# Performance work log

Hardware: AMD Instinct MI355X
Metric: run time of the kernel (lower is better)

The kernel has to match this reference:

```python
import jax, jax.numpy as jnp
import numpy as np
from jax import lax

EPS = 1e-06
QP_ITERS = 500  # unrolled mirror-descent iterations for the simplex QP


def mlp_embed(x, W1, b1, W2, b2):
    # embedding_net: 2-layer MLP, [B, N, in_dim] -> [B, N, embed_dim]
    h = jax.nn.relu(jnp.einsum('bni,ih->bnh', x, W1) + b1)
    return jnp.einsum('bnh,hd->bnd', h, W2) + b2


def batch_svdd(emb, eps):
    # emb: [B, S, D].  SVDD dual QP per task:
    #   min_a  a^T K a - diag(K)^T a   s.t.  a >= 0, sum(a) = 1
    # (Q = 2K, p = -diag(K), G = -I, h = 0, A = 1^T, b = 1 in the torch QPFunction call)
    B, S, D = emb.shape
    K = jnp.einsum('bsd,btd->bst', emb, emb) + eps * jnp.eye(S, dtype=emb.dtype)
    kdiag = jnp.diagonal(K, axis1=-2, axis2=-1)  # [B, S]
    # Solve on the simplex with exponentiated-gradient (mirror descent with KL),
    # which converges to the unique QP optimum (K is PD after the eps jitter).
    # Per-task step size from the Gershgorin bound: eta <= 1 / (2 * ||K||_inf).
    eta = 1.0 / (2.0 * jnp.max(jnp.sum(jnp.abs(K), axis=-1), axis=-1, keepdims=True))  # [B,1]
    a0 = jnp.full((B, S), 1.0 / S, dtype=emb.dtype)

    def step(a, _):
        g = 2.0 * jnp.einsum('bst,bt->bs', K, a) - kdiag  # grad of a^T K a - kdiag^T a
        a = jax.nn.softmax(jnp.log(a + 1e-30) - eta * g, axis=-1)
        return a, None

    alphas, _ = lax.scan(step, a0, None, length=QP_ITERS)
    centers = jnp.einsum('bs,bsd->bd', alphas, emb)  # sum(alphas * inputs, dim=1)
    return centers


def setup_inputs() -> dict:
    key = jax.random.key(0)
    ks = jax.random.split(key, 4)
    tasks, shot, n_query, in_dim, hid, emb = 256, 32, 64, 1024, 2048, 512
    support_inputs = jax.random.normal(ks[0], (tasks, shot, in_dim), jnp.float32)
    query_inputs = jax.random.normal(ks[1], (tasks, n_query, in_dim), jnp.float32)
    W1 = jax.random.normal(ks[2], (in_dim, hid), jnp.float32) / np.sqrt(in_dim)
    b1 = jnp.zeros((hid,), jnp.float32)
    W2 = jax.random.normal(ks[3], (hid, emb), jnp.float32) / np.sqrt(hid)
    b2 = jnp.zeros((emb,), jnp.float32)
    return {'support_inputs': support_inputs, 'query_inputs': query_inputs,
            'W1': W1, 'b1': b1, 'W2': W2, 'b2': b2}


def reference(support_inputs, query_inputs, W1, b1, W2, b2):
    support_emb = mlp_embed(support_inputs, W1, b1, W2, b2)  # [B, S, D]
    centers = batch_svdd(support_emb, EPS)                   # [B, D]
    query_emb = mlp_embed(query_inputs, W1, b1, W2, b2)      # [B, Q, D]
    logits = -jnp.sum((centers[:, None, :] - query_emb) ** 2, axis=-1)  # [B, Q]
    return logits
```

## Files before the change

kernel.cpp:

```cpp
#include <hip/hip_runtime.h>
#include <hip/hip_bf16.h>

typedef __attribute__((ext_vector_type(8))) short bf16x8;
typedef __attribute__((ext_vector_type(4))) float f32x4;
typedef __attribute__((ext_vector_type(4))) unsigned short us4;

__device__ __forceinline__ unsigned short bf16_rne(float f) {
  unsigned u = __float_as_uint(f);
  unsigned r = u + 0x7fffu + ((u >> 16) & 1u);
  return (unsigned short)(r >> 16);
}

__device__ __forceinline__ void gload16(const void* g, void* l) {
  typedef const __attribute__((address_space(1))) unsigned int* gas;
  typedef __attribute__((address_space(3))) unsigned int* las;
  __builtin_amdgcn_global_load_lds((gas)g, (las)l, 16, 0, 0);
}

__device__ __forceinline__ float lane_f(float v, int l) {
  return __int_as_float(__builtin_amdgcn_readlane(__float_as_int(v), l));
}

template <int CTRL>
__device__ __forceinline__ float dpp_add(float x) {
  return x + __int_as_float(__builtin_amdgcn_update_dpp(0, __float_as_int(x), CTRL, 0xf, 0xf, true));
}

#define BAR() asm volatile("s_barrier" ::: "memory")
#define VMCNT0() asm volatile("s_waitcnt vmcnt(0)" ::: "memory")
#define LGKM4() asm volatile("s_waitcnt lgkmcnt(4)" ::: "memory")
#define LGKM0() asm volatile("s_waitcnt lgkmcnt(0)" ::: "memory")
#define SB() __builtin_amdgcn_sched_barrier(0)

__global__ __launch_bounds__(256) void castx(const float* __restrict__ sup,
                                             const float* __restrict__ qry,
                                             unsigned short* __restrict__ X) {
  const int stride = gridDim.x * blockDim.x;
  for (int i = blockIdx.x * blockDim.x + threadIdx.x; i < 6291456; i += stride) {
    float4 v = (i < 2097152) ? ((const float4*)sup)[i] : ((const float4*)qry)[i - 2097152];
    us4 o = { bf16_rne(v.x), bf16_rne(v.y), bf16_rne(v.z), bf16_rne(v.w) };
    *(us4*)(X + (size_t)i * 4) = o;
  }
}

__global__ __launch_bounds__(256) void transcast(const float* __restrict__ src,
                                                 unsigned short* __restrict__ dst,
                                                 int R, int C) {
  __shared__ float t[32][33];
  const int tx = threadIdx.x & 31, ty = threadIdx.x >> 5;
  const int c0 = blockIdx.x * 32, r0 = blockIdx.y * 32;
#pragma unroll
  for (int j = 0; j < 4; j++)
    t[ty + j * 8][tx] = src[(size_t)(r0 + ty + j * 8) * C + c0 + tx];
  __syncthreads();
#pragma unroll
  for (int j = 0; j < 4; j++)
    dst[(size_t)(c0 + ty + j * 8) * R + r0 + tx] = bf16_rne(t[tx][ty + j * 8]);
}

#define MFMA_Q(AO, BO, MOFF, NOFF)                                                  \
  __builtin_amdgcn_s_setprio(1);                                                    \
  _Pragma("unroll") for (int i_ = 0; i_ < 4; ++i_)                                  \
  _Pragma("unroll") for (int j_ = 0; j_ < 2; ++j_)                                  \
  _Pragma("unroll") for (int ks_ = 0; ks_ < 2; ++ks_)                               \
    acc[(MOFF) + i_][(NOFF) + j_] = __builtin_amdgcn_mfma_f32_16x16x32_bf16(        \
        AO[i_][ks_], BO[j_][ks_], acc[(MOFF) + i_][(NOFF) + j_], 0, 0, 0);          \
  __builtin_amdgcn_s_setprio(0);

#define RDA(KS, ACH, MH, I) \
  (*(const bf16x8*)(lsc + ((ACH) * 32768 + (MH) * 8192 + (I) * 2048) + ((KS) ? vA_1 : vA_0)))
#define RDB(KS, BCH, JI) \
  (*(const bf16x8*)(lsc + ((BCH) * 32768 + (JI) * 2048) + ((KS) ? vB_1 : vB_0)))

#define STG(GLP, CHOFF, HALF)                                                     \
  gload16((GLP) + (size_t)((HALF) * 128) * ld,                                    \
          (char*)ls + ((CHOFF) + (HALF) * 16384) + wid * 1024);                   \
  gload16((GLP) + (size_t)((HALF) * 128 + 64) * ld,                               \
          (char*)ls + ((CHOFF) + (HALF) * 16384 + 8192) + wid * 1024);

#define TILE(ACH, BCH, ASO, BSO, T)                                               \
  {                                                                               \
    VMCNT0();                                                                     \
    BAR();                                                                        \
    _Pragma("unroll") for (int i = 0; i < 4; ++i) {                               \
      afr[i][0] = RDA(0, ACH, 0, i); afr[i][1] = RDA(1, ACH, 0, i);               \
    }                                                                             \
    _Pragma("unroll") for (int j = 0; j < 2; ++j) {                               \
      bfr0[j][0] = RDB(0, BCH, j); bfr0[j][1] = RDB(1, BCH, j);                   \
    }                                                                             \
    _Pragma("unroll") for (int j = 0; j < 2; ++j) {                               \
      bfr1[j][0] = RDB(0, BCH, 2 + j); bfr1[j][1] = RDB(1, BCH, 2 + j);           \
    }                                                                             \
    const char* Ap_ = AgL + (size_t)(T) * 128;                                    \
    const char* Bp_ = BgL + (size_t)(T) * 128;                                    \
    STG(Ap_, ASO, 0); STG(Ap_, ASO, 1);                                           \
    STG(Bp_, BSO, 0); STG(Bp_, BSO, 1);                                           \
    LGKM4(); SB();                                                                \
    MFMA_Q(afr, bfr0, 0, 0);                                                      \
    LGKM0(); SB();                                                                \
    MFMA_Q(afr, bfr1, 0, 2);                                                      \
    _Pragma("unroll") for (int i = 0; i < 4; ++i) {                               \
      afr[i][0] = RDA(0, ACH, 1, i); afr[i][1] = RDA(1, ACH, 1, i);               \
    }                                                                             \
    LGKM0(); SB();                                                                \
    MFMA_Q(afr, bfr1, 4, 2);                                                      \
    MFMA_Q(afr, bfr0, 4, 0);                                                      \
  }

template <int ACT, int OUTBF>
__global__ __launch_bounds__(512) void gemm256(const unsigned short* __restrict__ A,
                                               const unsigned short* __restrict__ BT,
                                               const float* __restrict__ bias,
                                               void* __restrict__ Cout,
                                               int M, int N, int K) {
  __shared__ __attribute__((aligned(16))) short ls[4][16384];
  const int tid = threadIdx.x, lane = tid & 63, wid = tid >> 6;
  const int wm = wid >> 2, wn = wid & 3;
  const int l15 = lane & 15, lg = lane >> 4;

  int lin = blockIdx.y * gridDim.x + blockIdx.x;
  int nwg = gridDim.x * gridDim.y;
  int swz = (lin & 7) * (nwg >> 3) + (lin >> 3);
  int bx = swz % gridDim.x, by = swz / gridDim.x;
  const int m0 = by * 256, n0 = bx * 256;

  const size_t ld = (size_t)K * 2;
  const char* Ag = (const char*)A + (size_t)m0 * ld;
  const char* Bg = (const char*)BT + (size_t)n0 * ld;
  const int NT = K >> 6;
  const char* lsc = (const char*)ls;

  const int swz4 = (l15 & 7) << 4;
  const int bk0 = (l15 * 128 + lg * 16) ^ swz4;
  const int bk1 = (l15 * 128 + 64 + lg * 16) ^ swz4;
  const int vA_0 = bk0 + wm * 16384, vA_1 = bk1 + wm * 16384;
  const int vB_0 = bk0 + wn * 8192 + 65536, vB_1 = bk1 + wn * 8192 + 65536;

  const int srow = wid * 8 + (lane >> 3);
  const int kperm = ((lane & 7) ^ (lane >> 3)) << 4;
  const char* AgL = Ag + (size_t)srow * ld + kperm;
  const char* BgL = Bg + (size_t)srow * ld + kperm;

  f32x4 acc[8][4] = {};
  bf16x8 afr[4][2], bfr0[2][2], bfr1[2][2];

  STG(AgL, 0, 0); STG(AgL, 0, 1);
  STG(BgL, 65536, 0); STG(BgL, 65536, 1);

  for (int u = 0; u < NT; u += 2) {
    int t1 = u + 1;
    int t2 = u + 2; if (t2 >= NT) t2 = 0;
    TILE(0, 0, 32768, 98304, t1);
    TILE(1, 1, 0, 65536, t2);
  }

  float bv[4];
#pragma unroll
  for (int nf = 0; nf < 4; ++nf) bv[nf] = bias[n0 + wn * 64 + nf * 16 + l15];
#pragma unroll
  for (int mf = 0; mf < 8; ++mf) {
    int rbase = m0 + wm * 128 + mf * 16 + lg * 4;
#pragma unroll
    for (int nf = 0; nf < 4; ++nf) {
      int col = n0 + wn * 64 + nf * 16 + l15;
#pragma unroll
      for (int j = 0; j < 4; ++j) {
        float v = acc[mf][nf][j] + bv[nf];
        if (ACT) v = v > 0.f ? v : 0.f;
        size_t idx = (size_t)(rbase + j) * N + col;
        if (OUTBF) ((unsigned short*)Cout)[idx] = bf16_rne(v);
        else       ((float*)Cout)[idx] = v;
      }
    }
  }
}

template <int ACT, int OUTBF, int K>
__global__ __launch_bounds__(256, 3) void gemm2(const unsigned short* __restrict__ A,
                                                const unsigned short* __restrict__ BT,
                                                const float* __restrict__ bias,
                                                void* __restrict__ Cout,
                                                int N) {
  __shared__ __attribute__((aligned(16))) short ls[4][4096];
  const int tid = threadIdx.x, lane = tid & 63, wid = tid >> 6;
  const int wm = wid >> 1, wn = wid & 1;
  const int l15 = lane & 15, lg = lane >> 4;

  int lin = blockIdx.y * gridDim.x + blockIdx.x;
  int nwg = gridDim.x * gridDim.y;
  int swz = (lin & 7) * (nwg >> 3) + (lin >> 3);
  int bx = swz % gridDim.x, by = swz / gridDim.x;
  const int m0 = by * 128, n0 = bx * 128;

  constexpr size_t ldb = (size_t)K * 2;
  constexpr int NT = K >> 5;
  const char* Ag = (const char*)A + (size_t)m0 * ldb;
  const char* Bg = (const char*)BT + (size_t)n0 * ldb;
  char* lsw = (char*)ls;
  const char* lsc = (const char*)ls;

  const int vbase = l15 * 64 + ((lg ^ (l15 & 3)) << 4);
  const int vA = vbase + wm * 4096;
  const int vB = vbase + wn * 4096 + 16384;

  const int srow = wid * 16 + (lane >> 2);
  const int kperm = ((lane & 3) ^ ((lane >> 2) & 3)) << 4;
  const char* AgL = Ag + (size_t)srow * ldb + kperm;
  const char* BgL = Bg + (size_t)srow * ldb + kperm;

  f32x4 acc[4][4] = {};
  bf16x8 afr[4], bfr[4];

  auto STAGE = [&](const char* gl, int choff, int t) {
    gload16(gl + (size_t)t * 64, lsw + choff + wid * 1024);
    gload16(gl + 64 * ldb + (size_t)t * 64, lsw + choff + 4096 + wid * 1024);
  };

  auto TILE2 = [&](int ch, int oc, int tst) {
    VMCNT0();
    BAR();
#pragma unroll
    for (int i = 0; i < 4; ++i)
      afr[i] = *(const bf16x8*)(lsc + ch * 4096 + i * 1024 + vA);
#pragma unroll
    for (int nf = 0; nf < 4; ++nf)
      bfr[nf] = *(const bf16x8*)(lsc + ch * 4096 + nf * 1024 + vB);
    STAGE(AgL, oc * 4096, tst);
    STAGE(BgL, 16384 + oc * 4096, tst);
    __builtin_amdgcn_s_setprio(1);
#pragma unroll
    for (int nf = 0; nf < 4; ++nf)
#pragma unroll
      for (int i = 0; i < 4; ++i)
        acc[i][nf] = __builtin_amdgcn_mfma_f32_16x16x32_bf16(afr[i], bfr[nf],
                                                             acc[i][nf], 0, 0, 0);
    __builtin_amdgcn_s_setprio(0);
  };

  STAGE(AgL, 0, 0);
  STAGE(BgL, 16384, 0);
  for (int u = 0; u < NT; u += 2) {
    int t2 = u + 2; if (t2 >= NT) t2 = 0;
    TILE2(0, 1, u + 1);
    TILE2(1, 0, t2);
  }

  float bv[4];
#pragma unroll
  for (int nf = 0; nf < 4; ++nf) bv[nf] = bias[n0 + wn * 64 + nf * 16 + l15];
#pragma unroll
  for (int i = 0; i < 4; ++i) {
    int rbase = m0 + wm * 64 + i * 16 + lg * 4;
#pragma unroll
    for (int nf = 0; nf < 4; ++nf) {
      int col = n0 + wn * 64 + nf * 16 + l15;
#pragma unroll
      for (int j = 0; j < 4; ++j) {
        float v = acc[i][nf][j] + bv[nf];
        if (ACT) v = v > 0.f ? v : 0.f;
        size_t idx = (size_t)(rbase + j) * N + col;
        if (OUTBF) ((unsigned short*)Cout)[idx] = bf16_rne(v);
        else       ((float*)Cout)[idx] = v;
      }
    }
  }
}

__global__ __launch_bounds__(256) void makeK(const float* __restrict__ E,
                                             float* __restrict__ Km,
                                             float* __restrict__ eta2v) {
  __shared__ float es[32][512];
  const int b = blockIdx.x, tid = threadIdx.x;
  const float4* Eb = (const float4*)(E + (size_t)b * 32 * 512);
  float4* es4 = (float4*)&es[0][0];
  for (int i = tid; i < 32 * 128; i += 256) es4[i] = Eb[i];
  __syncthreads();

  const int s = tid >> 3, tq = tid & 7;
  const float4* rs4 = (const float4*)&es[s][0];
  const float4* rt0 = (const float4*)&es[tq * 4 + 0][0];
  const float4* rt1 = (const float4*)&es[tq * 4 + 1][0];
  const float4* rt2 = (const float4*)&es[tq * 4 + 2][0];
  const float4* rt3 = (const float4*)&es[tq * 4 + 3][0];
  float4 a0 = {0, 0, 0, 0}, a1 = {0, 0, 0, 0}, a2 = {0, 0, 0, 0}, a3 = {0, 0, 0, 0};
  for (int dd = 0; dd < 128; ++dd) {
    float4 av = rs4[dd];
    float4 b0 = rt0[dd], b1 = rt1[dd], b2 = rt2[dd], b3 = rt3[dd];
    a0.x = fmaf(av.x, b0.x, a0.x); a0.y = fmaf(av.y, b0.y, a0.y);
    a0.z = fmaf(av.z, b0.z, a0.z); a0.w = fmaf(av.w, b0.w, a0.w);
    a1.x = fmaf(av.x, b1.x, a1.x); a1.y = fmaf(av.y, b1.y, a1.y);
    a1.z = fmaf(av.z, b1.z, a1.z); a1.w = fmaf(av.w, b1.w, a1.w);
    a2.x = fmaf(av.x, b2.x, a2.x); a2.y = fmaf(av.y, b2.y, a2.y);
    a2.z = fmaf(av.z, b2.z, a2.z); a2.w = fmaf(av.w, b2.w, a2.w);
    a3.x = fmaf(av.x, b3.x, a3.x); a3.y = fmaf(av.y, b3.y, a3.y);
    a3.z = fmaf(av.z, b3.z, a3.z); a3.w = fmaf(av.w, b3.w, a3.w);
  }
  float kv[4] = { (a0.x + a0.y) + (a0.z + a0.w), (a1.x + a1.y) + (a1.z + a1.w),
                  (a2.x + a2.y) + (a2.z + a2.w), (a3.x + a3.y) + (a3.z + a3.w) };
  float p = 0.f;
#pragma unroll
  for (int j = 0; j < 4; j++) {
    if (s == tq * 4 + j) kv[j] += 1e-6f;
    p += fabsf(kv[j]);
    Km[(size_t)b * 1024 + s * 32 + tq * 4 + j] = kv[j];
  }
  p += __shfl_xor(p, 1); p += __shfl_xor(p, 2); p += __shfl_xor(p, 4);
  __syncthreads();
  float* rs = &es[0][0];
  if (tq == 0) rs[s] = p;
  __syncthreads();
  if (tid < 32) {
    float m = rs[tid];
    m = fmaxf(m, __shfl_xor(m, 1));
    m = fmaxf(m, __shfl_xor(m, 2));
    m = fmaxf(m, __shfl_xor(m, 4));
    m = fmaxf(m, __shfl_xor(m, 8));
    m = fmaxf(m, __shfl_xor(m, 16));
    if (tid == 0) eta2v[b] = 1.4426950408889634f / (2.0f * m);
  }
}

__global__ __launch_bounds__(256) void qp_kernel(const float* __restrict__ Km,
                                                 const float* __restrict__ eta2v,
                                                 float* __restrict__ alp) {
  const int lane = threadIdx.x & 63, wid = threadIdx.x >> 6;
  const int b = blockIdx.x * 4 + wid;
  const int s = lane & 31;
  const float* Kb = Km + (size_t)b * 1024;
  float kr[32];
#pragma unroll
  for (int i = 0; i < 8; i++) {
    float4 v = ((const float4*)(Kb + s * 32))[i];
    kr[i * 4 + 0] = v.x; kr[i * 4 + 1] = v.y; kr[i * 4 + 2] = v.z; kr[i * 4 + 3] = v.w;
  }
  const float kd = Kb[s * 33];
  const float eta2 = eta2v[b];
  const float c2p = fmaf(eta2, kd, 1.0f);
  const float m4n = -4.0f * eta2;
  float w = 0.03125f;
  for (int it = 0; it < 500; ++it) {
    float c0 = 0.f, c1 = 0.f, c2 = 0.f, c3 = 0.f, c4 = 0.f, c5 = 0.f, c6 = 0.f, c7 = 0.f;
#pragma unroll
    for (int t = 0; t < 4; ++t) {
      c0 = fmaf(kr[t],      lane_f(w, t),      c0);
      c1 = fmaf(kr[4 + t],  lane_f(w, 4 + t),  c1);
      c2 = fmaf(kr[8 + t],  lane_f(w, 8 + t),  c2);
      c3 = fmaf(kr[12 + t], lane_f(w, 12 + t), c3);
      c4 = fmaf(kr[16 + t], lane_f(w, 16 + t), c4);
      c5 = fmaf(kr[20 + t], lane_f(w, 20 + t), c5);
      c6 = fmaf(kr[24 + t], lane_f(w, 24 + t), c6);
      c7 = fmaf(kr[28 + t], lane_f(w, 28 + t), c7);
    }
    float tK = (((c0 + c1) + (c2 + c3)) + ((c4 + c5) + (c6 + c7)));
    float r = w;
    r = dpp_add<0x128>(r);
    r = dpp_add<0x124>(r);
    r = dpp_add<0x122>(r);
    r = dpp_add<0x121>(r);
    r = dpp_add<0x142>(r);
    r = dpp_add<0x143>(r);
    float R2 = __builtin_amdgcn_rcpf(lane_f(r, 63));
    float z = fmaf(m4n * R2, tK, c2p);
    w = (w * R2) * __builtin_amdgcn_exp2f(z);
  }
  float r = w;
  r = dpp_add<0x128>(r);
  r = dpp_add<0x124>(r);
  r = dpp_add<0x122>(r);
  r = dpp_add<0x121>(r);
  r = dpp_add<0x142>(r);
  r = dpp_add<0x143>(r);
  float R2 = __builtin_amdgcn_rcpf(lane_f(r, 63));
  if (lane < 32) alp[(size_t)b * 32 + s] = 2.0f * w * R2;
}

__global__ __launch_bounds__(128) void centers_k(const float* __restrict__ alp,
                                                 const float* __restrict__ E,
                                                 float* __restrict__ ctr) {
  const int b = blockIdx.x, t = threadIdx.x;
  __shared__ float av[32];
  if (t < 32) av[t] = alp[(size_t)b * 32 + t];
  __syncthreads();
  const float4* Eb = (const float4*)(E + (size_t)b * 32 * 512);
  float4 c = {0, 0, 0, 0};
#pragma unroll 8
  for (int sIdx = 0; sIdx < 32; sIdx++) {
    float a = av[sIdx];
    float4 v = Eb[sIdx * 128 + t];
    c.x = fmaf(a, v.x, c.x); c.y = fmaf(a, v.y, c.y);
    c.z = fmaf(a, v.z, c.z); c.w = fmaf(a, v.w, c.w);
  }
  ((float4*)ctr)[b * 128 + t] = c;
}

__global__ __launch_bounds__(256) void logits_k(const float* __restrict__ ctr,
                                                const float* __restrict__ E,
                                                float* __restrict__ out) {
  const int b = blockIdx.x, lane = threadIdx.x & 63, w = threadIdx.x >> 6;
  const float4* C4 = (const float4*)(ctr + (size_t)b * 512);
  const float4 cA = C4[lane * 2], cB = C4[lane * 2 + 1];
  const float4* Q4 = (const float4*)(E + (size_t)(8192 + b * 64) * 512);
  for (int q = w; q < 64; q += 4) {
    float4 e0 = Q4[(size_t)q * 128 + lane * 2];
    float4 e1 = Q4[(size_t)q * 128 + lane * 2 + 1];
    float d, ss = 0.f;
    d = cA.x - e0.x; ss = fmaf(d, d, ss);
    d = cA.y - e0.y; ss = fmaf(d, d, ss);
    d = cA.z - e0.z; ss = fmaf(d, d, ss);
    d = cA.w - e0.w; ss = fmaf(d, d, ss);
    d = cB.x - e1.x; ss = fmaf(d, d, ss);
    d = cB.y - e1.y; ss = fmaf(d, d, ss);
    d = cB.z - e1.z; ss = fmaf(d, d, ss);
    d = cB.w - e1.w; ss = fmaf(d, d, ss);
    ss += __shfl_xor(ss, 1);  ss += __shfl_xor(ss, 2);  ss += __shfl_xor(ss, 4);
    ss += __shfl_xor(ss, 8);  ss += __shfl_xor(ss, 16); ss += __shfl_xor(ss, 32);
    if (lane == 0) out[b * 64 + q] = -ss;
  }
}

extern "C" void kernel_launch(void* const* d_in, const int* in_sizes, int n_in,
                              void* d_out, int out_size, void* d_ws, size_t ws_size,
                              hipStream_t stream) {
  const float* sup = (const float*)d_in[0];
  const float* qry = (const float*)d_in[1];
  const float* W1  = (const float*)d_in[2];
  const float* b1  = (const float*)d_in[3];
  const float* W2  = (const float*)d_in[4];
  const float* b2  = (const float*)d_in[5];
  float* out = (float*)d_out;

  char* ws = (char*)d_ws;
  unsigned short* H   = (unsigned short*)(ws);
  unsigned short* Xbf = (unsigned short*)(ws + 100663296);
  float* E    = (float*)(ws + 100663296);
  unsigned short* W1T = (unsigned short*)(ws + 150994944);
  unsigned short* W2T = (unsigned short*)(ws + 155189248);
  float* Km   = (float*)(ws + 157286400);
  float* eta2 = (float*)(ws + 158334976);
  float* alp  = (float*)(ws + 158336000);
  float* ctr  = (float*)(ws + 158368768);

  castx<<<dim3(2048), dim3(256), 0, stream>>>(sup, qry, Xbf);
  transcast<<<dim3(64, 32), dim3(256), 0, stream>>>(W1, W1T, 1024, 2048);
  transcast<<<dim3(16, 64), dim3(256), 0, stream>>>(W2, W2T, 2048, 512);
  gemm256<1, 1><<<dim3(8, 96), dim3(512), 0, stream>>>(Xbf, W1T, b1, (void*)H, 24576, 2048, 1024);
  gemm2<0, 0, 2048><<<dim3(4, 192), dim3(256), 0, stream>>>(H, W2T, b2, (void*)E, 512);
  makeK<<<dim3(256), dim3(256), 0, stream>>>(E, Km, eta2);
  qp_kernel<<<dim3(64), dim3(256), 0, stream>>>(Km, eta2, alp);
  centers_k<<<dim3(256), dim3(128), 0, stream>>>(alp, E, ctr);
  logits_k<<<dim3(256), dim3(256), 0, stream>>>(ctr, E, out);
}
```

Measured before the change: 311.4 us.

## Retile second GEMM to full-N 64-row tiles and use LDS broadcast in QP

The second MLP GEMM now gives each block a 64x512 output tile spanning the whole N dimension, with 128 columns per wave. Each row of H is therefore loaded once instead of once per N tile, at the cost of more LDS, more accumulator registers and only two blocks per CU. The QP kernel writes the iterate to LDS and reads it back as float4 broadcasts, splitting the 32-term dot product across both half-waves and combining them with a shuffle. This replaces 32 readlanes per iteration. The castx launch grid is also doubled.

```diff
diff --git a/kernel.cpp b/kernel.cpp
--- a/kernel.cpp
+++ b/kernel.cpp
@@ -175,45 +175,43 @@
   }
 }
 
-template <int ACT, int OUTBF, int K>
-__global__ __launch_bounds__(256, 3) void gemm2(const unsigned short* __restrict__ A,
+template <int K>
+__global__ __launch_bounds__(256, 2) void gemm2(const unsigned short* __restrict__ A,
                                                 const unsigned short* __restrict__ BT,
                                                 const float* __restrict__ bias,
-                                                void* __restrict__ Cout,
+                                                float* __restrict__ Cout,
                                                 int N) {
-  __shared__ __attribute__((aligned(16))) short ls[4][4096];
+  __shared__ __attribute__((aligned(16))) short ls[2][18432];
   const int tid = threadIdx.x, lane = tid & 63, wid = tid >> 6;
-  const int wm = wid >> 1, wn = wid & 1;
   const int l15 = lane & 15, lg = lane >> 4;
 
-  int lin = blockIdx.y * gridDim.x + blockIdx.x;
-  int nwg = gridDim.x * gridDim.y;
+  int lin = blockIdx.x;
+  int nwg = gridDim.x;
   int swz = (lin & 7) * (nwg >> 3) + (lin >> 3);
-  int bx = swz % gridDim.x, by = swz / gridDim.x;
-  const int m0 = by * 128, n0 = bx * 128;
+  const int m0 = swz * 64;
 
   constexpr size_t ldb = (size_t)K * 2;
   constexpr int NT = K >> 5;
   const char* Ag = (const char*)A + (size_t)m0 * ldb;
-  const char* Bg = (const char*)BT + (size_t)n0 * ldb;
+  const char* Bg = (const char*)BT;
   char* lsw = (char*)ls;
   const char* lsc = (const char*)ls;
 
-  const int vbase = l15 * 64 + ((lg ^ (l15 & 3)) << 4);
-  const int vA = vbase + wm * 4096;
-  const int vB = vbase + wn * 4096 + 16384;
-
-  const int srow = wid * 16 + (lane >> 2);
+  const int vb = l15 * 64 + ((lg ^ (l15 & 3)) << 4);
+
   const int kperm = ((lane & 3) ^ ((lane >> 2) & 3)) << 4;
-  const char* AgL = Ag + (size_t)srow * ldb + kperm;
-  const char* BgL = Bg + (size_t)srow * ldb + kperm;
-
-  f32x4 acc[4][4] = {};
-  bf16x8 afr[4], bfr[4];
-
-  auto STAGE = [&](const char* gl, int choff, int t) {
-    gload16(gl + (size_t)t * 64, lsw + choff + wid * 1024);
-    gload16(gl + 64 * ldb + (size_t)t * 64, lsw + choff + 4096 + wid * 1024);
+  const char* AgL = Ag + (size_t)(wid * 16 + (lane >> 2)) * ldb + kperm;
+  const char* BgL = Bg + (size_t)(wid * 128 + (lane >> 2)) * ldb + kperm;
+
+  f32x4 acc[4][8] = {};
+  bf16x8 afr[4], bfr[8];
+
+  auto STAGE = [&](int buf, int t) {
+    gload16(AgL + (size_t)t * 64, lsw + buf * 36864 + wid * 1024);
+#pragma unroll
+    for (int q = 0; q < 8; ++q)
+      gload16(BgL + (size_t)(q * 16) * ldb + (size_t)t * 64,
+              lsw + buf * 36864 + 4096 + wid * 8192 + q * 1024);
   };
 
   auto TILE2 = [&](int ch, int oc, int tst) {
@@ -221,15 +219,14 @@
     BAR();
 #pragma unroll
     for (int i = 0; i < 4; ++i)
-      afr[i] = *(const bf16x8*)(lsc + ch * 4096 + i * 1024 + vA);
-#pragma unroll
-    for (int nf = 0; nf < 4; ++nf)
-      bfr[nf] = *(const bf16x8*)(lsc + ch * 4096 + nf * 1024 + vB);
-    STAGE(AgL, oc * 4096, tst);
-    STAGE(BgL, 16384 + oc * 4096, tst);
+      afr[i] = *(const bf16x8*)(lsc + ch * 36864 + i * 1024 + vb);
+#pragma unroll
+    for (int nf = 0; nf < 8; ++nf)
+      bfr[nf] = *(const bf16x8*)(lsc + ch * 36864 + 4096 + wid * 8192 + nf * 1024 + vb);
+    STAGE(oc, tst);
     __builtin_amdgcn_s_setprio(1);
 #pragma unroll
-    for (int nf = 0; nf < 4; ++nf)
+    for (int nf = 0; nf < 8; ++nf)
 #pragma unroll
       for (int i = 0; i < 4; ++i)
         acc[i][nf] = __builtin_amdgcn_mfma_f32_16x16x32_bf16(afr[i], bfr[nf],
@@ -237,31 +234,25 @@
     __builtin_amdgcn_s_setprio(0);
   };
 
-  STAGE(AgL, 0, 0);
-  STAGE(BgL, 16384, 0);
+  STAGE(0, 0);
   for (int u = 0; u < NT; u += 2) {
     int t2 = u + 2; if (t2 >= NT) t2 = 0;
     TILE2(0, 1, u + 1);
     TILE2(1, 0, t2);
   }
 
-  float bv[4];
-#pragma unroll
-  for (int nf = 0; nf < 4; ++nf) bv[nf] = bias[n0 + wn * 64 + nf * 16 + l15];
+  float bv[8];
+#pragma unroll
+  for (int nf = 0; nf < 8; ++nf) bv[nf] = bias[wid * 128 + nf * 16 + l15];
 #pragma unroll
   for (int i = 0; i < 4; ++i) {
-    int rbase = m0 + wm * 64 + i * 16 + lg * 4;
-#pragma unroll
-    for (int nf = 0; nf < 4; ++nf) {
-      int col = n0 + wn * 64 + nf * 16 + l15;
-#pragma unroll
-      for (int j = 0; j < 4; ++j) {
-        float v = acc[i][nf][j] + bv[nf];
-        if (ACT) v = v > 0.f ? v : 0.f;
-        size_t idx = (size_t)(rbase + j) * N + col;
-        if (OUTBF) ((unsigned short*)Cout)[idx] = bf16_rne(v);
-        else       ((float*)Cout)[idx] = v;
-      }
+    int rbase = m0 + i * 16 + lg * 4;
+#pragma unroll
+    for (int nf = 0; nf < 8; ++nf) {
+      int col = wid * 128 + nf * 16 + l15;
+#pragma unroll
+      for (int j = 0; j < 4; ++j)
+        Cout[(size_t)(rbase + j) * N + col] = acc[i][nf][j] + bv[nf];
     }
   }
 }
@@ -323,35 +314,25 @@
 __global__ __launch_bounds__(256) void qp_kernel(const float* __restrict__ Km,
                                                  const float* __restrict__ eta2v,
                                                  float* __restrict__ alp) {
+  __shared__ float wl[4][32];
   const int lane = threadIdx.x & 63, wid = threadIdx.x >> 6;
   const int b = blockIdx.x * 4 + wid;
-  const int s = lane & 31;
+  const int s = lane & 31, h = lane >> 5;
   const float* Kb = Km + (size_t)b * 1024;
-  float kr[32];
-#pragma unroll
-  for (int i = 0; i < 8; i++) {
-    float4 v = ((const float4*)(Kb + s * 32))[i];
+  float kr[16];
+#pragma unroll
+  for (int i = 0; i < 4; i++) {
+    float4 v = ((const float4*)(Kb + s * 32 + h * 16))[i];
     kr[i * 4 + 0] = v.x; kr[i * 4 + 1] = v.y; kr[i * 4 + 2] = v.z; kr[i * 4 + 3] = v.w;
   }
   const float kd = Kb[s * 33];
   const float eta2 = eta2v[b];
   const float c2p = fmaf(eta2, kd, 1.0f);
   const float m4n = -4.0f * eta2;
+  const float4* wv = (const float4*)&wl[wid][h * 16];
   float w = 0.03125f;
   for (int it = 0; it < 500; ++it) {
-    float c0 = 0.f, c1 = 0.f, c2 = 0.f, c3 = 0.f, c4 = 0.f, c5 = 0.f, c6 = 0.f, c7 = 0.f;
-#pragma unroll
-    for (int t = 0; t < 4; ++t) {
-      c0 = fmaf(kr[t],      lane_f(w, t),      c0);
-      c1 = fmaf(kr[4 + t],  lane_f(w, 4 + t),  c1);
-      c2 = fmaf(kr[8 + t],  lane_f(w, 8 + t),  c2);
-      c3 = fmaf(kr[12 + t], lane_f(w, 12 + t), c3);
-      c4 = fmaf(kr[16 + t], lane_f(w, 16 + t), c4);
-      c5 = fmaf(kr[20 + t], lane_f(w, 20 + t), c5);
-      c6 = fmaf(kr[24 + t], lane_f(w, 24 + t), c6);
-      c7 = fmaf(kr[28 + t], lane_f(w, 28 + t), c7);
-    }
-    float tK = (((c0 + c1) + (c2 + c3)) + ((c4 + c5) + (c6 + c7)));
+    wl[wid][s] = w;
     float r = w;
     r = dpp_add<0x128>(r);
     r = dpp_add<0x124>(r);
@@ -360,6 +341,18 @@
     r = dpp_add<0x142>(r);
     r = dpp_add<0x143>(r);
     float R2 = __builtin_amdgcn_rcpf(lane_f(r, 63));
+    float4 q0 = wv[0], q1 = wv[1], q2 = wv[2], q3 = wv[3];
+    float c0 = 0.f, c1 = 0.f, c2 = 0.f, c3 = 0.f;
+    c0 = fmaf(kr[0],  q0.x, c0); c0 = fmaf(kr[1],  q0.y, c0);
+    c0 = fmaf(kr[2],  q0.z, c0); c0 = fmaf(kr[3],  q0.w, c0);
+    c1 = fmaf(kr[4],  q1.x, c1); c1 = fmaf(kr[5],  q1.y, c1);
+    c1 = fmaf(kr[6],  q1.z, c1); c1 = fmaf(kr[7],  q1.w, c1);
+    c2 = fmaf(kr[8],  q2.x, c2); c2 = fmaf(kr[9],  q2.y, c2);
+    c2 = fmaf(kr[10], q2.z, c2); c2 = fmaf(kr[11], q2.w, c2);
+    c3 = fmaf(kr[12], q3.x, c3); c3 = fmaf(kr[13], q3.y, c3);
+    c3 = fmaf(kr[14], q3.z, c3); c3 = fmaf(kr[15], q3.w, c3);
+    float half = (c0 + c1) + (c2 + c3);
+    float tK = half + __shfl_xor(half, 32);
     float z = fmaf(m4n * R2, tK, c2p);
     w = (w * R2) * __builtin_amdgcn_exp2f(z);
   }
@@ -440,11 +433,11 @@
   float* alp  = (float*)(ws + 158336000);
   float* ctr  = (float*)(ws + 158368768);
 
-  castx<<<dim3(2048), dim3(256), 0, stream>>>(sup, qry, Xbf);
+  castx<<<dim3(4096), dim3(256), 0, stream>>>(sup, qry, Xbf);
   transcast<<<dim3(64, 32), dim3(256), 0, stream>>>(W1, W1T, 1024, 2048);
   transcast<<<dim3(16, 64), dim3(256), 0, stream>>>(W2, W2T, 2048, 512);
   gemm256<1, 1><<<dim3(8, 96), dim3(512), 0, stream>>>(Xbf, W1T, b1, (void*)H, 24576, 2048, 1024);
-  gemm2<0, 0, 2048><<<dim3(4, 192), dim3(256), 0, stream>>>(H, W2T, b2, (void*)E, 512);
+  gemm2<2048><<<dim3(384), dim3(256), 0, stream>>>(H, W2T, b2, E, 512);
   makeK<<<dim3(256), dim3(256), 0, stream>>>(E, Km, eta2);
   qp_kernel<<<dim3(64), dim3(256), 0, stream>>>(Km, eta2, alp);
   centers_k<<<dim3(256), dim3(128), 0, stream>>>(alp, E, ctr);
```

New measurement: 341.5 us. 9.7% more time.

## Replace second-layer GEMM with 192x256 tile, 512-thread kernel using 64-wide K steps

Applied to the files above, without the earlier changes.

The H×W2 GEMM (24576×512×2048) moves from 128×128 tiles with 256 threads and 32-wide K chunks to 192×256 tiles with 512 threads (8 waves, 2×4) and 64-wide K chunks with XOR-swizzled LDS. The larger tile raises arithmetic intensity per LDS and global byte and halves the K-loop barrier count. The grid becomes exactly 256 workgroups, one per CU on the device. Fragment loads are split so MFMAs on the first B half can start while the remaining LDS reads are outstanding. In exchange it uses about 112 KB of LDS and many more accumulator registers per wave, which limits occupancy to one block per CU.

```diff
diff --git a/kernel.cpp b/kernel.cpp
--- a/kernel.cpp
+++ b/kernel.cpp
@@ -175,93 +175,119 @@
   }
 }
 
-template <int ACT, int OUTBF, int K>
-__global__ __launch_bounds__(256, 3) void gemm2(const unsigned short* __restrict__ A,
-                                                const unsigned short* __restrict__ BT,
-                                                const float* __restrict__ bias,
-                                                void* __restrict__ Cout,
-                                                int N) {
-  __shared__ __attribute__((aligned(16))) short ls[4][4096];
+#define MFMA_T(AO, BO, MOFF, NOFF)                                                  \
+  __builtin_amdgcn_s_setprio(1);                                                    \
+  _Pragma("unroll") for (int i_ = 0; i_ < 3; ++i_)                                  \
+  _Pragma("unroll") for (int j_ = 0; j_ < 2; ++j_)                                  \
+  _Pragma("unroll") for (int ks_ = 0; ks_ < 2; ++ks_)                               \
+    acc[(MOFF) + i_][(NOFF) + j_] = __builtin_amdgcn_mfma_f32_16x16x32_bf16(        \
+        AO[i_][ks_], BO[j_][ks_], acc[(MOFF) + i_][(NOFF) + j_], 0, 0, 0);          \
+  __builtin_amdgcn_s_setprio(0);
+
+#define RA2(KS, ACH, MH, I) \
+  (*(const bf16x8*)(lsc + ((ACH) * 24576 + (MH) * 6144 + (I) * 2048) + ((KS) ? vA_1 : vA_0)))
+#define RB2(KS, BCH, JI) \
+  (*(const bf16x8*)(lsc + ((BCH) * 32768 + (JI) * 2048) + ((KS) ? vB_1 : vB_0)))
+
+#define STGA2(CHOFF, T)                                                           \
+  {                                                                               \
+    const char* p_ = AgL + (size_t)(T) * 128;                                     \
+    gload16(p_,               (char*)ls + (CHOFF) + wid * 3072);                  \
+    gload16(p_ + 8 * ld,      (char*)ls + (CHOFF) + wid * 3072 + 1024);           \
+    gload16(p_ + 16 * ld,     (char*)ls + (CHOFF) + wid * 3072 + 2048);           \
+  }
+#define STGB2(CHOFF, T)                                                           \
+  {                                                                               \
+    const char* p_ = BgL + (size_t)(T) * 128;                                     \
+    gload16(p_,               (char*)ls + (CHOFF) + wid * 4096);                  \
+    gload16(p_ + 8 * ld,      (char*)ls + (CHOFF) + wid * 4096 + 1024);           \
+    gload16(p_ + 16 * ld,     (char*)ls + (CHOFF) + wid * 4096 + 2048);           \
+    gload16(p_ + 24 * ld,     (char*)ls + (CHOFF) + wid * 4096 + 3072);           \
+  }
+
+#define TILE2(ACH, BCH, ASO, BSO, T)                                              \
+  {                                                                               \
+    VMCNT0();                                                                     \
+    BAR();                                                                        \
+    _Pragma("unroll") for (int i = 0; i < 3; ++i) {                               \
+      afl[i][0] = RA2(0, ACH, 0, i); afl[i][1] = RA2(1, ACH, 0, i);               \
+    }                                                                             \
+    _Pragma("unroll") for (int j = 0; j < 2; ++j) {                               \
+      bfr0[j][0] = RB2(0, BCH, j); bfr0[j][1] = RB2(1, BCH, j);                   \
+    }                                                                             \
+    _Pragma("unroll") for (int j = 0; j < 2; ++j) {                               \
+      bfr1[j][0] = RB2(0, BCH, 2 + j); bfr1[j][1] = RB2(1, BCH, 2 + j);           \
+    }                                                                             \
+    STGA2(ASO, T); STGB2(BSO, T);                                                 \
+    LGKM4(); SB();                                                                \
+    MFMA_T(afl, bfr0, 0, 0);                                                      \
+    LGKM0(); SB();                                                                \
+    MFMA_T(afl, bfr1, 0, 2);                                                      \
+    _Pragma("unroll") for (int i = 0; i < 3; ++i) {                               \
+      afl[i][0] = RA2(0, ACH, 1, i); afl[i][1] = RA2(1, ACH, 1, i);               \
+    }                                                                             \
+    LGKM0(); SB();                                                                \
+    MFMA_T(afl, bfr1, 3, 2);                                                      \
+    MFMA_T(afl, bfr0, 3, 0);                                                      \
+  }
+
+__global__ __launch_bounds__(512) void gemm192(const unsigned short* __restrict__ A,
+                                               const unsigned short* __restrict__ BT,
+                                               const float* __restrict__ bias,
+                                               float* __restrict__ Cout) {
+  __shared__ __attribute__((aligned(16))) short ls[57344];
   const int tid = threadIdx.x, lane = tid & 63, wid = tid >> 6;
-  const int wm = wid >> 1, wn = wid & 1;
+  const int wm = wid >> 2, wn = wid & 3;
   const int l15 = lane & 15, lg = lane >> 4;
 
   int lin = blockIdx.y * gridDim.x + blockIdx.x;
   int nwg = gridDim.x * gridDim.y;
   int swz = (lin & 7) * (nwg >> 3) + (lin >> 3);
   int bx = swz % gridDim.x, by = swz / gridDim.x;
-  const int m0 = by * 128, n0 = bx * 128;
-
-  constexpr size_t ldb = (size_t)K * 2;
-  constexpr int NT = K >> 5;
-  const char* Ag = (const char*)A + (size_t)m0 * ldb;
-  const char* Bg = (const char*)BT + (size_t)n0 * ldb;
-  char* lsw = (char*)ls;
+  const int m0 = by * 192, n0 = bx * 256;
+
+  constexpr int K = 2048;
+  const size_t ld = (size_t)K * 2;
+  const char* Ag = (const char*)A + (size_t)m0 * ld;
+  const char* Bg = (const char*)BT + (size_t)n0 * ld;
+  constexpr int NT = K >> 6;
   const char* lsc = (const char*)ls;
 
-  const int vbase = l15 * 64 + ((lg ^ (l15 & 3)) << 4);
-  const int vA = vbase + wm * 4096;
-  const int vB = vbase + wn * 4096 + 16384;
-
-  const int srow = wid * 16 + (lane >> 2);
-  const int kperm = ((lane & 3) ^ ((lane >> 2) & 3)) << 4;
-  const char* AgL = Ag + (size_t)srow * ldb + kperm;
-  const char* BgL = Bg + (size_t)srow * ldb + kperm;
-
-  f32x4 acc[4][4] = {};
-  bf16x8 afr[4], bfr[4];
-
-  auto STAGE = [&](const char* gl, int choff, int t) {
-    gload16(gl + (size_t)t * 64, lsw + choff + wid * 1024);
-    gload16(gl + 64 * ldb + (size_t)t * 64, lsw + choff + 4096 + wid * 1024);
-  };
-
-  auto TILE2 = [&](int ch, int oc, int tst) {
-    VMCNT0();
-    BAR();
-#pragma unroll
-    for (int i = 0; i < 4; ++i)
-      afr[i] = *(const bf16x8*)(lsc + ch * 4096 + i * 1024 + vA);
-#pragma unroll
-    for (int nf = 0; nf < 4; ++nf)
-      bfr[nf] = *(const bf16x8*)(lsc + ch * 4096 + nf * 1024 + vB);
-    STAGE(AgL, oc * 4096, tst);
-    STAGE(BgL, 16384 + oc * 4096, tst);
-    __builtin_amdgcn_s_setprio(1);
-#pragma unroll
-    for (int nf = 0; nf < 4; ++nf)
-#pragma unroll
-      for (int i = 0; i < 4; ++i)
-        acc[i][nf] = __builtin_amdgcn_mfma_f32_16x16x32_bf16(afr[i], bfr[nf],
-                                                             acc[i][nf], 0, 0, 0);
-    __builtin_amdgcn_s_setprio(0);
-  };
-
-  STAGE(AgL, 0, 0);
-  STAGE(BgL, 16384, 0);
+  const int swz4 = (l15 & 7) << 4;
+  const int bk0 = (l15 * 128 + lg * 16) ^ swz4;
+  const int bk1 = (l15 * 128 + 64 + lg * 16) ^ swz4;
+  const int vA_0 = bk0 + wm * 12288, vA_1 = bk1 + wm * 12288;
+  const int vB_0 = bk0 + wn * 8192 + 49152, vB_1 = bk1 + wn * 8192 + 49152;
+
+  const int kperm = ((lane & 7) ^ (lane >> 3)) << 4;
+  const char* AgL = Ag + (size_t)(wid * 24 + (lane >> 3)) * ld + kperm;
+  const char* BgL = Bg + (size_t)(wid * 32 + (lane >> 3)) * ld + kperm;
+
+  f32x4 acc[6][4] = {};
+  bf16x8 afl[3][2], bfr0[2][2], bfr1[2][2];
+
+  STGA2(0, 0);
+  STGB2(49152, 0);
+
   for (int u = 0; u < NT; u += 2) {
+    int t1 = u + 1;
     int t2 = u + 2; if (t2 >= NT) t2 = 0;
-    TILE2(0, 1, u + 1);
-    TILE2(1, 0, t2);
+    TILE2(0, 0, 24576, 81920, t1);
+    TILE2(1, 1, 0, 49152, t2);
   }
 
   float bv[4];
 #pragma unroll
   for (int nf = 0; nf < 4; ++nf) bv[nf] = bias[n0 + wn * 64 + nf * 16 + l15];
 #pragma unroll
-  for (int i = 0; i < 4; ++i) {
-    int rbase = m0 + wm * 64 + i * 16 + lg * 4;
+  for (int mf = 0; mf < 6; ++mf) {
+    int rbase = m0 + wm * 96 + mf * 16 + lg * 4;
 #pragma unroll
     for (int nf = 0; nf < 4; ++nf) {
       int col = n0 + wn * 64 + nf * 16 + l15;
 #pragma unroll
-      for (int j = 0; j < 4; ++j) {
-        float v = acc[i][nf][j] + bv[nf];
-        if (ACT) v = v > 0.f ? v : 0.f;
-        size_t idx = (size_t)(rbase + j) * N + col;
-        if (OUTBF) ((unsigned short*)Cout)[idx] = bf16_rne(v);
-        else       ((float*)Cout)[idx] = v;
-      }
+      for (int j = 0; j < 4; ++j)
+        Cout[(size_t)(rbase + j) * 512 + col] = acc[mf][nf][j] + bv[nf];
     }
   }
 }
@@ -444,7 +470,7 @@
   transcast<<<dim3(64, 32), dim3(256), 0, stream>>>(W1, W1T, 1024, 2048);
   transcast<<<dim3(16, 64), dim3(256), 0, stream>>>(W2, W2T, 2048, 512);
   gemm256<1, 1><<<dim3(8, 96), dim3(512), 0, stream>>>(Xbf, W1T, b1, (void*)H, 24576, 2048, 1024);
-  gemm2<0, 0, 2048><<<dim3(4, 192), dim3(256), 0, stream>>>(H, W2T, b2, (void*)E, 512);
+  gemm192<<<dim3(2, 128), dim3(512), 0, stream>>>(H, W2T, b2, E);
   makeK<<<dim3(256), dim3(256), 0, stream>>>(E, Km, eta2);
   qp_kernel<<<dim3(64), dim3(256), 0, stream>>>(Km, eta2, alp);
   centers_k<<<dim3(256), dim3(128), 0, stream>>>(alp, E, ctr);
```

New measurement: 298.6 us, median of 3. -4.1%, faster.
